# Performance work log

Hardware: AMD Instinct MI355X
Metric: run time of the kernel (lower is better)

The kernel has to match this reference:

```python
import jax, jax.numpy as jnp
import numpy as np
from jax import lax

BITWIDTH = 7
EPS = 1e-5


def ti_quant(x):
    """TiFloatToInt8: per-tensor int8 quantization with power-of-2 scale."""
    rng = jnp.max(jnp.abs(x))
    bw = jnp.ceil(jnp.log2(rng))
    exp = bw - BITWIDTH
    q = jnp.clip(jnp.round(x * 2.0 ** (BITWIDTH - bw)), -128.0, 127.0)
    return q, exp


def ti_conv(xv, xe, wv, we, pad):
    """TiConv2d: integer conv (simulated in f32, all values int-valued),
    int32 accumulate, then shift back to 8 bits; exponents add."""
    acc = lax.conv_general_dilated(
        xv, wv, window_strides=(1, 1), padding=[(pad, pad), (pad, pad)],
        dimension_numbers=("NCHW", "OIHW", "NCHW"))
    rng = jnp.max(jnp.abs(acc))
    bw = jnp.ceil(jnp.log2(rng))
    shift = jnp.maximum(bw - BITWIDTH, 0.0)
    q = jnp.clip(jnp.round(acc * 2.0 ** (-shift)), -128.0, 127.0)
    return q, xe + we + shift


def batchnorm(x, gamma, beta):
    # training-mode BN: batch statistics over (N, H, W)
    mean = jnp.mean(x, axis=(0, 2, 3), keepdims=True)
    var = jnp.var(x, axis=(0, 2, 3), keepdims=True)
    g = gamma[None, :, None, None]
    b = beta[None, :, None, None]
    return g * (x - mean) * lax.rsqrt(var + EPS) + b


def setup_inputs() -> dict:
    key = jax.random.key(0)
    k0, k1, k2, k3, k4 = jax.random.split(key, 5)
    B, Cin, Cout, H, W = 32, 128, 256, 56, 56
    x_val = jax.random.randint(k0, (B, Cin, H, W), -128, 128, dtype=jnp.int32)
    x_exp = jnp.zeros((), jnp.float32) - 7.0
    wDW = jnp.round(jnp.clip(jax.random.normal(k1, (Cin, Cin, 3, 3), jnp.float32) * 32.0, -128.0, 127.0))
    wDW_exp = jnp.zeros((), jnp.float32) - 9.0
    wPW = jnp.round(jnp.clip(jax.random.normal(k2, (Cout, Cin, 1, 1), jnp.float32) * 32.0, -128.0, 127.0))
    wPW_exp = jnp.zeros((), jnp.float32) - 9.0
    gamma1 = jnp.ones((Cin,), jnp.float32) + 0.1 * jax.random.normal(k3, (Cin,), jnp.float32)
    beta1 = jnp.zeros((Cin,), jnp.float32)
    gamma2 = jnp.ones((Cout,), jnp.float32) + 0.1 * jax.random.normal(k4, (Cout,), jnp.float32)
    beta2 = jnp.zeros((Cout,), jnp.float32)
    return {"x_val": x_val, "x_exp": x_exp, "wDW": wDW, "wDW_exp": wDW_exp,
            "wPW": wPW, "wPW_exp": wPW_exp, "gamma1": gamma1, "beta1": beta1,
            "gamma2": gamma2, "beta2": beta2}


def reference(x_val, x_exp, wDW, wDW_exp, wPW, wPW_exp, gamma1, beta1, gamma2, beta2):
    xv = x_val.astype(jnp.float32)
    # convDW (3x3, in->in, pad=1)
    q, e = ti_conv(xv, x_exp, wDW, wDW_exp, 1)
    # dequant -> bn1 -> quant
    f = batchnorm(q * 2.0 ** e, gamma1, beta1)
    q, e = ti_quant(f)
    # TiReLU on int values
    q = jnp.maximum(q, 0.0)
    # convPW (1x1, in->out)
    q, e = ti_conv(q, e, wPW, wPW_exp, 0)
    # dequant -> bn2 -> quant -> relu
    f = batchnorm(q * 2.0 ** e, gamma2, beta2)
    q, e = ti_quant(f)
    q = jnp.maximum(q, 0.0)
    return q.astype(jnp.int8), e
```

## Files before the change

### kernel.cpp

```cpp
#include <hip/hip_runtime.h>
#include <cstdint>
#include <cstddef>

#define C1 128
#define C2 256
#define Hh 56
#define Wd 56
#define HW 3136
#define NHW 100352
#define N1 ((size_t)12845056)
#define N2 ((size_t)25690112)
#define XPSZ ((size_t)13778944)

typedef int v4i __attribute__((ext_vector_type(4)));
typedef int v16i __attribute__((ext_vector_type(16)));

static constexpr size_t OFF_XP = 0;
static constexpr size_t OFF_ACC1 = XPSZ;
static constexpr size_t OFF_Q1 = OFF_ACC1 + 4 * N1;
static constexpr size_t OFF_Q3 = OFF_Q1 + N1;
static constexpr size_t OFF_WQ1 = OFF_Q3 + N2;
static constexpr size_t OFF_WQ2 = OFF_WQ1 + 147456;
static constexpr size_t OFF_STATS = OFF_WQ2 + 32768;

struct Stats {
  int absmax1, absmax2, pad0, pad1;
  float scale1, e1, s2, e2;
  float scaleq2, e3, sf, ef;
  int sum1[C1]; unsigned sumsq1[C1];
  int min1[C1], max1[C1];
  int sum2[C2]; unsigned sumsq2[C2];
  int min2[C2], max2[C2];
};

__global__ __launch_bounds__(256) void k_prep_all(
    const float* __restrict__ wDW, const float* __restrict__ wPW,
    signed char* __restrict__ wq1t, signed char* __restrict__ wq2t, Stats* st) {
  int b = blockIdx.x, t = threadIdx.x;
  if (b < 576) {
    int idx = b * 256 + t;
    int co = idx / 1152, r = idx - co * 1152;
    int ci = r / 9, pos = r - ci * 9;
    int k = pos * 128 + ci;
    wq1t[(size_t)(k >> 4) * 2048 + co * 16 + (k & 15)] = (signed char)(int)wDW[idx];
  } else if (b < 704) {
    int i = (b - 576) * 256 + t;
    int co = i >> 7, ci = i & 127;
    wq2t[(size_t)(ci >> 4) * 4096 + co * 16 + (ci & 15)] = (signed char)(int)wPW[i];
  } else {
    if (t == 0) { st->absmax1 = 0; st->absmax2 = 0; }
    for (int c = t; c < C1; c += 256) {
      st->sum1[c] = 0; st->sumsq1[c] = 0; st->min1[c] = 127; st->max1[c] = -128;
    }
    for (int c = t; c < C2; c += 256) {
      st->sum2[c] = 0; st->sumsq2[c] = 0; st->min2[c] = 127; st->max2[c] = -128;
    }
  }
}

__global__ __launch_bounds__(256) void k_prep_x2(
    const int* __restrict__ x, signed char* __restrict__ xp) {
  __shared__ signed char lds[56 * 132];
  int t = threadIdx.x;
  int hh = blockIdx.x;
  int n = blockIdx.y;
  int* xpw = (int*)(xp + ((size_t)n * 58 + hh) * 7424);
  if (hh == 0 || hh == 57) {
    for (int o = t; o < 1856; o += 256) xpw[o] = 0;
    return;
  }
  int h = hh - 1;
  const int* xb = x + (size_t)n * C1 * HW + h * 56;
  for (int idx = t; idx < 7168; idx += 256) {
    int c = idx / 56, w = idx - c * 56;
    lds[w * 132 + c] = (signed char)xb[(size_t)c * HW + w];
  }
  __syncthreads();
  for (int o = t; o < 1856; o += 256) {
    int kb = o / 232, r = o - kb * 232, ww = r >> 2, cw = r & 3;
    int val = (ww == 0 || ww == 57) ? 0
              : *(const int*)&lds[(ww - 1) * 132 + kb * 16 + cw * 4];
    xpw[o] = val;
  }
}

__device__ inline v4i ld16_lds(const signed char* p) {
  const int2* q = (const int2*)p;
  int2 lo = q[0], hi = q[1];
  v4i r; r[0] = lo.x; r[1] = lo.y; r[2] = hi.x; r[3] = hi.y;
  return r;
}

__global__ __launch_bounds__(256, 4) void k_conv1s(
    const signed char* __restrict__ xp, const signed char* __restrict__ wq1t,
    int* __restrict__ acc1, Stats* st) {
  __shared__ int reda[4];
  int t = threadIdx.x, lane = t & 63, wave = t >> 6;
  int half = lane >> 5, l31 = lane & 31;
  int mw = wave & 1, nw = wave >> 1;
  size_t g0 = (size_t)blockIdx.x * 128;

  const signed char* ab[2];
#pragma unroll
  for (int i = 0; i < 2; ++i) {
    size_t gm = g0 + mw * 64 + i * 32 + l31;
    int n = (int)(gm / HW);
    int p = (int)(gm - (size_t)n * HW);
    int h = p / 56, w = p - h * 56;
    ab[i] = xp + ((size_t)n * 58 + h) * 7424 + w * 16 + half * 928;
  }
  const signed char* bb[2];
#pragma unroll
  for (int j = 0; j < 2; ++j)
    bb[j] = wq1t + (size_t)(nw * 64 + j * 32 + l31) * 16 + half * 2048;

  v16i a1[2][2];
#pragma unroll
  for (int i = 0; i < 2; ++i)
#pragma unroll
    for (int j = 0; j < 2; ++j)
#pragma unroll
      for (int r = 0; r < 16; ++r) a1[i][j][r] = 0;

#pragma unroll
  for (int pos = 0; pos < 9; ++pos) {
    int kh = pos / 3, kw = pos - kh * 3;
    const signed char* a0p = ab[0] + kh * 7424 + kw * 16;
    const signed char* a1p = ab[1] + kh * 7424 + kw * 16;
#pragma unroll
    for (int kb = 0; kb < 8; kb += 2) {
      v4i af0 = *(const v4i*)(a0p + kb * 928);
      v4i af1 = *(const v4i*)(a1p + kb * 928);
      v4i bf0 = *(const v4i*)(bb[0] + pos * 16384 + kb * 2048);
      v4i bf1 = *(const v4i*)(bb[1] + pos * 16384 + kb * 2048);
      a1[0][0] = __builtin_amdgcn_mfma_i32_32x32x32_i8(af0, bf0, a1[0][0], 0, 0, 0);
      a1[0][1] = __builtin_amdgcn_mfma_i32_32x32x32_i8(af0, bf1, a1[0][1], 0, 0, 0);
      a1[1][0] = __builtin_amdgcn_mfma_i32_32x32x32_i8(af1, bf0, a1[1][0], 0, 0, 0);
      a1[1][1] = __builtin_amdgcn_mfma_i32_32x32x32_i8(af1, bf1, a1[1][1], 0, 0, 0);
    }
  }

  int am = 0;
#pragma unroll
  for (int i = 0; i < 2; ++i)
#pragma unroll
    for (int j = 0; j < 2; ++j)
#pragma unroll
      for (int r = 0; r < 16; ++r) am = max(am, abs(a1[i][j][r]));
  for (int off = 32; off; off >>= 1) am = max(am, __shfl_down(am, off, 64));
  if (lane == 0) reda[wave] = am;
  __syncthreads();
  if (t == 0)
    atomicMax(&st->absmax1, max(max(reda[0], reda[1]), max(reda[2], reda[3])));

  int* ob = acc1 + (size_t)blockIdx.x * 16384;
#pragma unroll
  for (int i = 0; i < 2; ++i)
#pragma unroll
    for (int j = 0; j < 2; ++j)
#pragma unroll
      for (int reg = 0; reg < 16; ++reg)
        ob[(((wave * 2 + i) * 2 + j) * 16 + reg) * 64 + lane] = a1[i][j][reg];
}

__global__ __launch_bounds__(256, 4) void k_qstats1(
    const int* __restrict__ acc1, signed char* __restrict__ q1, Stats* st,
    const float* __restrict__ x_exp, const float* __restrict__ wDW_exp) {
  __shared__ int qti[128 * 34];
  __shared__ int psum[C1], psq[C1], pmn[C1], pmx[C1];
  signed char* qt = (signed char*)qti;
  int t = threadIdx.x, lane = t & 63, wave = t >> 6;
  int half = lane >> 5, l31 = lane & 31;
  int mw = wave & 1, nw = wave >> 1;

  if (t < C1) { psum[t] = 0; psq[t] = 0; pmn[t] = 127; pmx[t] = -128; }
  __syncthreads();

  int v1 = st->absmax1;
  int pw = 31 - __clz(v1 | 1);
  int bw = ((v1 & (v1 - 1)) == 0) ? pw : pw + 1;
  int sh = max(bw - 7, 0);
  float scale1 = exp2f((float)(-sh));
  if (blockIdx.x == 0 && t == 0)
    st->e1 = x_exp[0] + wDW_exp[0] + (float)sh;

  const int* ib = acc1 + (size_t)blockIdx.x * 16384;
#pragma unroll
  for (int j = 0; j < 2; ++j) {
    int sj = 0, sqj = 0, mnj = 127, mxj = -128;
    int c = nw * 64 + j * 32 + l31;
#pragma unroll
    for (int i = 0; i < 2; ++i)
#pragma unroll
      for (int reg = 0; reg < 16; ++reg) {
        int av = ib[(((wave * 2 + i) * 2 + j) * 16 + reg) * 64 + lane];
        int row = (reg & 3) + 8 * (reg >> 2) + 4 * half;
        int pix = mw * 64 + i * 32 + row;
        float r = rintf((float)av * scale1);
        r = fminf(fmaxf(r, -128.f), 127.f);
        int qi = (int)r;
        qt[pix * 136 + c] = (signed char)qi;
        sj += qi; sqj += qi * qi; mnj = min(mnj, qi); mxj = max(mxj, qi);
      }
    sj += __shfl_down(sj, 32, 64);
    sqj += __shfl_down(sqj, 32, 64);
    mnj = min(mnj, __shfl_down(mnj, 32, 64));
    mxj = max(mxj, __shfl_down(mxj, 32, 64));
    if (half == 0) {
      atomicAdd(&psum[c], sj); atomicAdd(&psq[c], sqj);
      atomicMin(&pmn[c], mnj); atomicMax(&pmx[c], mxj);
    }
  }
  __syncthreads();
  if (t < C1) {
    atomicAdd(&st->sum1[t], psum[t]);
    atomicAdd(&st->sumsq1[t], (unsigned)psq[t]);
    atomicMin(&st->min1[t], pmn[t]);
    atomicMax(&st->max1[t], pmx[t]);
  }
  int* q1w = (int*)(q1 + (size_t)blockIdx.x * 128 * 128);
  for (int idx = t; idx < 4096; idx += 256) {
    int pix = idx >> 5, c4 = idx & 31;
    q1w[idx] = qti[pix * 34 + c4];
  }
}

template <int STORE>
__global__ __launch_bounds__(256, 2) void k_conv2t(
    const signed char* __restrict__ q1, const signed char* __restrict__ wq2t,
    signed char* __restrict__ q3, Stats* st,
    const float* __restrict__ gamma1, const float* __restrict__ beta1,
    const float* __restrict__ wPW_exp) {
  __shared__ int bufi[8448];
  __shared__ int psum[C2], psq[C2], pmn[C2], pmx[C2];
  __shared__ float bnA[C1], bnB[C1], redf[2];
  __shared__ int reda[4];
  signed char* qt = (signed char*)bufi;
  signed char* stg = (signed char*)bufi;

  int t = threadIdx.x, lane = t & 63, wave = t >> 6;
  int half = lane >> 5, l31 = lane & 31;
  size_t g0 = (size_t)blockIdx.x * 128;

  if (STORE) { psum[t] = 0; psq[t] = 0; pmn[t] = 127; pmx[t] = -128; }

  float e1 = st->e1;
  float cand = 0.f;
  if (t < C1) {
    double meanq = (double)st->sum1[t] / (double)NHW;
    double varq = (double)st->sumsq1[t] / (double)NHW - meanq * meanq;
    float se = exp2f(e1);
    float mean = (float)meanq * se;
    float var = (float)varq * se * se;
    float rsq = 1.0f / sqrtf(var + 1e-5f);
    float g = gamma1[t], b = beta1[t];
    float Avv = g * se * rsq;
    float Bvv = b - g * mean * rsq;
    bnA[t] = Avv; bnB[t] = Bvv;
    cand = fmaxf(fabsf(Avv * (float)st->min1[t] + Bvv),
                 fabsf(Avv * (float)st->max1[t] + Bvv));
  }
  if (wave < 2) {
    for (int off = 32; off; off >>= 1) cand = fmaxf(cand, __shfl_down(cand, off, 64));
    if (lane == 0) redf[wave] = cand;
  }
  __syncthreads();
  float rng = fmaxf(redf[0], redf[1]);
  float bwv = ceilf(log2f(rng));
  float s2 = exp2f(7.0f - bwv);
  float e2 = bwv - 7.0f;

  int c4 = t & 31;
  float Av[4], Bv[4];
#pragma unroll
  for (int jj = 0; jj < 4; ++jj) {
    Av[jj] = bnA[c4 * 4 + jj];
    Bv[jj] = bnB[c4 * 4 + jj];
  }
  const int* q1w = (const int*)(q1 + g0 * 128);
#pragma unroll
  for (int k = 0; k < 16; ++k) {
    int idx = k * 256 + t;
    int v = q1w[idx];
    int pix = idx >> 5;
    int outv = 0;
#pragma unroll
    for (int jj = 0; jj < 4; ++jj) {
      int b = (signed char)(v >> (8 * jj));
      float y = Av[jj] * (float)b + Bv[jj];
      float r = rintf(y * s2);
      r = fminf(fmaxf(r, -128.f), 127.f);
      r = fmaxf(r, 0.f);
      outv |= ((int)r & 0xff) << (8 * jj);
    }
    bufi[pix * 34 + c4] = outv;
  }
  __syncthreads();

  int am2 = 0;
  float scale2 = 0.f;
  int sh2 = 0;
  if (STORE) {
    int v2 = st->absmax2;
    int pw = 31 - __clz(v2 | 1);
    int bw = ((v2 & (v2 - 1)) == 0) ? pw : pw + 1;
    sh2 = max(bw - 7, 0);
    scale2 = exp2f((float)(-sh2));
    if (blockIdx.x == 0 && t == 0)
      st->e3 = e2 + wPW_exp[0] + (float)sh2;
  }
  int pq[2][4][4];
#pragma unroll
  for (int ch = 0; ch < 2; ++ch) {
    v16i acc[4];
#pragma unroll
    for (int j = 0; j < 4; ++j)
#pragma unroll
      for (int r = 0; r < 16; ++r) acc[j][r] = 0;
#pragma unroll
    for (int ks = 0; ks < 4; ++ks) {
      v4i af = ld16_lds(&qt[(wave * 32 + l31) * 136 + half * 16 + ks * 32]);
#pragma unroll
      for (int j = 0; j < 4; ++j) {
        v4i bf = *(const v4i*)(wq2t + (size_t)(ks * 2 + half) * 4096 +
                               (ch * 128 + j * 32 + l31) * 16);
        acc[j] = __builtin_amdgcn_mfma_i32_32x32x32_i8(af, bf, acc[j], 0, 0, 0);
      }
    }
    if (STORE == 0) {
#pragma unroll
      for (int j = 0; j < 4; ++j)
#pragma unroll
        for (int r = 0; r < 16; ++r) am2 = max(am2, abs(acc[j][r]));
    } else {
#pragma unroll
      for (int j = 0; j < 4; ++j) {
        int c = ch * 128 + j * 32 + l31;
        int sj = 0, sqj = 0, mnj = 127, mxj = -128;
        int pk[4] = {0, 0, 0, 0};
#pragma unroll
        for (int reg = 0; reg < 16; ++reg) {
          float r = rintf((float)acc[j][reg] * scale2);
          r = fminf(fmaxf(r, -128.f), 127.f);
          int qi = (int)r;
          pk[reg >> 2] |= (qi & 0xff) << ((reg & 3) * 8);
          sj += qi; sqj += qi * qi; mnj = min(mnj, qi); mxj = max(mxj, qi);
        }
#pragma unroll
        for (int k = 0; k < 4; ++k) pq[ch][j][k] = pk[k];
        sj += __shfl_down(sj, 32, 64);
        sqj += __shfl_down(sqj, 32, 64);
        mnj = min(mnj, __shfl_down(mnj, 32, 64));
        mxj = max(mxj, __shfl_down(mxj, 32, 64));
        if (half == 0) {
          atomicAdd(&psum[c], sj); atomicAdd(&psq[c], sqj);
          atomicMin(&pmn[c], mnj); atomicMax(&pmx[c], mxj);
        }
      }
    }
  }

  if (STORE == 0) {
    for (int off = 32; off; off >>= 1) am2 = max(am2, __shfl_down(am2, off, 64));
    if (lane == 0) reda[wave] = am2;
    __syncthreads();
    if (t == 0)
      atomicMax(&st->absmax2, max(max(reda[0], reda[1]), max(reda[2], reda[3])));
  } else {
    __syncthreads();
#pragma unroll
    for (int ch = 0; ch < 2; ++ch)
#pragma unroll
      for (int j = 0; j < 4; ++j)
#pragma unroll
        for (int k = 0; k < 4; ++k) {
          int word = pq[ch][j][k];
#pragma unroll
          for (int b = 0; b < 4; ++b) {
            int row = b + 8 * k + 4 * half;
            stg[(wave * 32 + row) * 264 + ch * 128 + j * 32 + l31] =
                (signed char)(word >> (8 * b));
          }
        }
    __syncthreads();
    atomicAdd(&st->sum2[t], psum[t]);
    atomicAdd(&st->sumsq2[t], (unsigned)psq[t]);
    atomicMin(&st->min2[t], pmn[t]);
    atomicMax(&st->max2[t], pmx[t]);
    int* q3w = (int*)(q3 + g0 * 256);
#pragma unroll
    for (int k = 0; k < 32; ++k) {
      int idx = k * 256 + t;
      int pix = idx >> 6, cw = idx & 63;
      q3w[idx] = *(const int*)&stg[pix * 264 + cw * 4];
    }
  }
}

__global__ __launch_bounds__(256) void k_out(
    const signed char* __restrict__ q3, const Stats* __restrict__ st,
    const float* __restrict__ gamma2, const float* __restrict__ beta2,
    float* __restrict__ out) {
  __shared__ signed char lds[64 * 260];
  __shared__ float bnA2[C2], bnB2[C2], redf2[4];
  int t = threadIdx.x, lane = t & 63, wave = t >> 6;
  size_t g0 = (size_t)blockIdx.x * 64;
  int n = (int)(g0 / HW), p0 = (int)(g0 - (size_t)n * HW);
  const int* q3w = (const int*)(q3 + g0 * 256);
#pragma unroll
  for (int k = 0; k < 16; ++k) {
    int idx = k * 256 + t;
    int pix = idx >> 6, cw = idx & 63;
    *(int*)&lds[pix * 260 + cw * 4] = q3w[idx];
  }
  float e3 = st->e3;
  {
    double meanq = (double)st->sum2[t] / (double)NHW;
    double varq = (double)st->sumsq2[t] / (double)NHW - meanq * meanq;
    float se = exp2f(e3);
    float mean = (float)meanq * se;
    float var = (float)varq * se * se;
    float rsq = 1.0f / sqrtf(var + 1e-5f);
    float g = gamma2[t], b = beta2[t];
    float Avv = g * se * rsq;
    float Bvv = b - g * mean * rsq;
    bnA2[t] = Avv; bnB2[t] = Bvv;
    float cand = fmaxf(fabsf(Avv * (float)st->min2[t] + Bvv),
                       fabsf(Avv * (float)st->max2[t] + Bvv));
    for (int off = 32; off; off >>= 1) cand = fmaxf(cand, __shfl_down(cand, off, 64));
    if (lane == 0) redf2[wave] = cand;
  }
  __syncthreads();
  float rng = fmaxf(fmaxf(redf2[0], redf2[1]), fmaxf(redf2[2], redf2[3]));
  float bwv = ceilf(log2f(rng));
  float sf = exp2f(7.0f - bwv);
  if (blockIdx.x == 0 && t == 0) out[N2] = bwv - 7.0f;

  float* ob = out + (size_t)n * C2 * HW + p0 + lane;
#pragma unroll
  for (int cg = 0; cg < 16; ++cg) {
    int v = *(const int*)&lds[lane * 260 + wave * 64 + cg * 4];
#pragma unroll
    for (int jj = 0; jj < 4; ++jj) {
      int c = wave * 64 + cg * 4 + jj;
      float y = bnA2[c] * (float)((signed char)(v >> (8 * jj))) + bnB2[c];
      float r = rintf(y * sf);
      r = fminf(fmaxf(r, -128.f), 127.f);
      ob[(size_t)c * HW] = fmaxf(r, 0.f);
    }
  }
}

extern "C" void kernel_launch(void* const* d_in, const int* in_sizes, int n_in,
                              void* d_out, int out_size, void* d_ws, size_t ws_size,
                              hipStream_t stream) {
  const int* x = (const int*)d_in[0];
  const float* x_exp = (const float*)d_in[1];
  const float* wDW = (const float*)d_in[2];
  const float* wDW_exp = (const float*)d_in[3];
  const float* wPW = (const float*)d_in[4];
  const float* wPW_exp = (const float*)d_in[5];
  const float* gamma1 = (const float*)d_in[6];
  const float* beta1 = (const float*)d_in[7];
  const float* gamma2 = (const float*)d_in[8];
  const float* beta2 = (const float*)d_in[9];
  float* out = (float*)d_out;

  char* ws = (char*)d_ws;
  signed char* xp2 = (signed char*)(ws + OFF_XP);
  int* acc1 = (int*)(ws + OFF_ACC1);
  signed char* q1 = (signed char*)(ws + OFF_Q1);
  signed char* q3 = (signed char*)(ws + OFF_Q3);
  signed char* wq1t = (signed char*)(ws + OFF_WQ1);
  signed char* wq2t = (signed char*)(ws + OFF_WQ2);
  Stats* st = (Stats*)(ws + OFF_STATS);

  hipLaunchKernelGGL(k_prep_all, dim3(705), dim3(256), 0, stream,
                     wDW, wPW, wq1t, wq2t, st);
  hipLaunchKernelGGL(k_prep_x2, dim3(58, 32), dim3(256), 0, stream, x, xp2);

  hipLaunchKernelGGL(k_conv1s, dim3(784), dim3(256), 0, stream,
                     xp2, wq1t, acc1, st);
  hipLaunchKernelGGL(k_qstats1, dim3(784), dim3(256), 0, stream,
                     acc1, q1, st, x_exp, wDW_exp);

  hipLaunchKernelGGL(k_conv2t<0>, dim3(784), dim3(256), 0, stream,
                     q1, wq2t, q3, st, gamma1, beta1, wPW_exp);
  hipLaunchKernelGGL(k_conv2t<1>, dim3(784), dim3(256), 0, stream,
                     q1, wq2t, q3, st, gamma1, beta1, wPW_exp);

  hipLaunchKernelGGL(k_out, dim3(1568), dim3(256), 0, stream,
                     q3, st, gamma2, beta2, out);
}
```

Measured before the change: 304.0 us.

## Merge input and weight prep kernels, add nontemporal loads/stores on streaming buffers

Folds the activation padding/transpose kernel into the weight-prep kernel so one launch does all preprocessing, removing a launch and its inter-kernel gap. Streaming global accesses (input read, acc1 write/read, q3 read, final output write) now use nontemporal builtins to reduce cache pollution. The merged kernel carries the LDS allocation for every block, which could reduce occupancy for the weight-only blocks, and nontemporal hints may hurt if any of that data would have been reused from L2/MALL.

After: 301.7 us. Within noise of the previous version (-0.8%).

```diff
diff --git a/kernel.cpp b/kernel.cpp
--- a/kernel.cpp
+++ b/kernel.cpp
@@ -33,18 +33,40 @@
   int min2[C2], max2[C2];
 };
 
-__global__ __launch_bounds__(256) void k_prep_all(
-    const float* __restrict__ wDW, const float* __restrict__ wPW,
+__global__ __launch_bounds__(256) void k_prep(
+    const int* __restrict__ x, const float* __restrict__ wDW,
+    const float* __restrict__ wPW, signed char* __restrict__ xp,
     signed char* __restrict__ wq1t, signed char* __restrict__ wq2t, Stats* st) {
+  __shared__ signed char lds[56 * 132];
   int b = blockIdx.x, t = threadIdx.x;
-  if (b < 576) {
-    int idx = b * 256 + t;
+  if (b < 1856) {
+    int hh = b % 58, n = b / 58;
+    int* xpw = (int*)(xp + ((size_t)n * 58 + hh) * 7424);
+    if (hh == 0 || hh == 57) {
+      for (int o = t; o < 1856; o += 256) xpw[o] = 0;
+      return;
+    }
+    int h = hh - 1;
+    const int* xb = x + (size_t)n * C1 * HW + h * 56;
+    for (int idx = t; idx < 7168; idx += 256) {
+      int c = idx / 56, w = idx - c * 56;
+      lds[w * 132 + c] = (signed char)__builtin_nontemporal_load(&xb[(size_t)c * HW + w]);
+    }
+    __syncthreads();
+    for (int o = t; o < 1856; o += 256) {
+      int kb = o / 232, r = o - kb * 232, ww = r >> 2, cw = r & 3;
+      int val = (ww == 0 || ww == 57) ? 0
+                : *(const int*)&lds[(ww - 1) * 132 + kb * 16 + cw * 4];
+      xpw[o] = val;
+    }
+  } else if (b < 2432) {
+    int idx = (b - 1856) * 256 + t;
     int co = idx / 1152, r = idx - co * 1152;
     int ci = r / 9, pos = r - ci * 9;
     int k = pos * 128 + ci;
     wq1t[(size_t)(k >> 4) * 2048 + co * 16 + (k & 15)] = (signed char)(int)wDW[idx];
-  } else if (b < 704) {
-    int i = (b - 576) * 256 + t;
+  } else if (b < 2560) {
+    int i = (b - 2432) * 256 + t;
     int co = i >> 7, ci = i & 127;
     wq2t[(size_t)(ci >> 4) * 4096 + co * 16 + (ci & 15)] = (signed char)(int)wPW[i];
   } else {
@@ -55,32 +77,6 @@
     for (int c = t; c < C2; c += 256) {
       st->sum2[c] = 0; st->sumsq2[c] = 0; st->min2[c] = 127; st->max2[c] = -128;
     }
-  }
-}
-
-__global__ __launch_bounds__(256) void k_prep_x2(
-    const int* __restrict__ x, signed char* __restrict__ xp) {
-  __shared__ signed char lds[56 * 132];
-  int t = threadIdx.x;
-  int hh = blockIdx.x;
-  int n = blockIdx.y;
-  int* xpw = (int*)(xp + ((size_t)n * 58 + hh) * 7424);
-  if (hh == 0 || hh == 57) {
-    for (int o = t; o < 1856; o += 256) xpw[o] = 0;
-    return;
-  }
-  int h = hh - 1;
-  const int* xb = x + (size_t)n * C1 * HW + h * 56;
-  for (int idx = t; idx < 7168; idx += 256) {
-    int c = idx / 56, w = idx - c * 56;
-    lds[w * 132 + c] = (signed char)xb[(size_t)c * HW + w];
-  }
-  __syncthreads();
-  for (int o = t; o < 1856; o += 256) {
-    int kb = o / 232, r = o - kb * 232, ww = r >> 2, cw = r & 3;
-    int val = (ww == 0 || ww == 57) ? 0
-              : *(const int*)&lds[(ww - 1) * 132 + kb * 16 + cw * 4];
-    xpw[o] = val;
   }
 }
 
@@ -160,7 +156,8 @@
     for (int j = 0; j < 2; ++j)
 #pragma unroll
       for (int reg = 0; reg < 16; ++reg)
-        ob[(((wave * 2 + i) * 2 + j) * 16 + reg) * 64 + lane] = a1[i][j][reg];
+        __builtin_nontemporal_store(
+            a1[i][j][reg], &ob[(((wave * 2 + i) * 2 + j) * 16 + reg) * 64 + lane]);
 }
 
 __global__ __launch_bounds__(256, 4) void k_qstats1(
@@ -193,7 +190,8 @@
     for (int i = 0; i < 2; ++i)
 #pragma unroll
       for (int reg = 0; reg < 16; ++reg) {
-        int av = ib[(((wave * 2 + i) * 2 + j) * 16 + reg) * 64 + lane];
+        int av = __builtin_nontemporal_load(
+            &ib[(((wave * 2 + i) * 2 + j) * 16 + reg) * 64 + lane]);
         int row = (reg & 3) + 8 * (reg >> 2) + 4 * half;
         int pix = mw * 64 + i * 32 + row;
         float r = rintf((float)av * scale1);
@@ -411,7 +409,7 @@
   for (int k = 0; k < 16; ++k) {
     int idx = k * 256 + t;
     int pix = idx >> 6, cw = idx & 63;
-    *(int*)&lds[pix * 260 + cw * 4] = q3w[idx];
+    *(int*)&lds[pix * 260 + cw * 4] = __builtin_nontemporal_load(&q3w[idx]);
   }
   float e3 = st->e3;
   {
@@ -446,7 +444,7 @@
       float y = bnA2[c] * (float)((signed char)(v >> (8 * jj))) + bnB2[c];
       float r = rintf(y * sf);
       r = fminf(fmaxf(r, -128.f), 127.f);
-      ob[(size_t)c * HW] = fmaxf(r, 0.f);
+      __builtin_nontemporal_store(fmaxf(r, 0.f), &ob[(size_t)c * HW]);
     }
   }
 }
@@ -475,9 +473,8 @@
   signed char* wq2t = (signed char*)(ws + OFF_WQ2);
   Stats* st = (Stats*)(ws + OFF_STATS);
 
-  hipLaunchKernelGGL(k_prep_all, dim3(705), dim3(256), 0, stream,
-                     wDW, wPW, wq1t, wq2t, st);
-  hipLaunchKernelGGL(k_prep_x2, dim3(58, 32), dim3(256), 0, stream, x, xp2);
+  hipLaunchKernelGGL(k_prep, dim3(2561), dim3(256), 0, stream,
+                     x, wDW, wPW, xp2, wq1t, wq2t, st);
 
   hipLaunchKernelGGL(k_conv1s, dim3(784), dim3(256), 0, stream,
                      xp2, wq1t, acc1, st);
```
